# Kernel optimization log

Measured on AMD Instinct MI355X. Metric: run time of the kernel, lower is better.

## Reference

```python
import jax, jax.numpy as jnp
import numpy as np

B, S, D = 8, 8192, 512
E, DFF = 16, 512
CAPACITY = 2


def setup_inputs() -> dict:
    key = jax.random.key(0)
    ks = jax.random.split(key, 4)
    x = jax.random.normal(ks[0], (B, S, D), dtype=jnp.float32)
    gate_weight = jax.random.normal(ks[1], (D, E), dtype=jnp.float32) * 0.006
    w1 = jax.random.normal(ks[2], (E, D, DFF), dtype=jnp.float32) * 0.02
    b1 = jnp.zeros((E, DFF), dtype=jnp.float32)
    w2 = jax.random.normal(ks[3], (E, DFF, D), dtype=jnp.float32) * 0.02
    b2 = jnp.zeros((E, D), dtype=jnp.float32)
    return {"x": x, "gate_weight": gate_weight, "w1": w1, "b1": b1, "w2": w2, "b2": b2}


def reference(x, gate_weight, w1, b1, w2, b2):
    Bx, Sx, Dx = x.shape
    num_experts = gate_weight.shape[1]
    k = Sx // num_experts * CAPACITY  # tokens per expert (capacity limit)

    # Router: softmax over experts, then each expert picks its top-k tokens.
    logits = jnp.einsum('bsd,de->bse', x, gate_weight)
    affinity = jax.nn.softmax(logits, axis=-1).transpose(0, 2, 1)  # [b, e, s]
    gating, index = jax.lax.top_k(affinity, k)  # [b, e, k] each

    # Dispatch: gather selected tokens per expert (== one-hot einsum in torch).
    x_in = jnp.take_along_axis(x[:, None, :, :], index[..., None], axis=2)  # [b, e, k, d]

    # Per-expert MLP (grouped GEMM over expert axis).
    h = jax.nn.gelu(jnp.einsum('bekd,edh->bekh', x_in, w1) + b1[None, :, None, :])
    x_e = jnp.einsum('bekh,ehd->bekd', h, w2) + b2[None, :, None, :]

    # Combine: weight by gate prob and scatter-add back to token positions.
    weighted = gating[..., None] * x_e  # [b, e, k, d]
    out = jnp.zeros_like(x)
    idx_flat = index.reshape(Bx, num_experts * k)
    vals_flat = weighted.reshape(Bx, num_experts * k, Dx)
    out = out.at[jnp.arange(Bx)[:, None], idx_flat].add(vals_flat)
    return out
```

## Files before the change

### kernel.cpp

```cpp
#include <hip/hip_runtime.h>
#include <hip/hip_bf16.h>

typedef __attribute__((ext_vector_type(8))) short short8;
typedef __attribute__((ext_vector_type(4))) float floatx4;
typedef __attribute__((ext_vector_type(4))) unsigned short ushort4_t;

#define B_    8
#define S_    8192
#define D_    512
#define E_    16
#define DFF_  512
#define KROW_ 1024

__device__ __forceinline__ float bf2f(unsigned short u) {
    return __uint_as_float(((unsigned int)u) << 16);
}
__device__ __forceinline__ unsigned short f2bf(float f) {
    unsigned int u = __float_as_uint(f);
    u += 0x7FFFu + ((u >> 16) & 1u);
    return (unsigned short)(u >> 16);
}
__device__ __forceinline__ float gelu_tanh(float v) {
    const float t = v * fmaf(0.0713548065f, v * v, 1.5957691216057308f);
    return v * __builtin_amdgcn_rcpf(1.0f + __expf(-t));
}

#define GLD16(g, l) __builtin_amdgcn_global_load_lds( \
    (const __attribute__((address_space(1))) void*)(g), \
    (__attribute__((address_space(3))) void*)(l), 16, 0, 0)

__global__ __launch_bounds__(256) void transpose_w_k(
    const float* __restrict__ w1, const float* __restrict__ w2,
    unsigned short* __restrict__ w1t, unsigned short* __restrict__ w2t)
{
    __shared__ unsigned short tile[32][33];
    const int e = blockIdx.z & 15;
    const float*    src = (blockIdx.z < 16) ? w1 : w2;
    unsigned short* dst = (blockIdx.z < 16) ? w1t : w2t;
    const int x0 = blockIdx.x * 32, y0 = blockIdx.y * 32;
    const int tx = threadIdx.x, ty = threadIdx.y;
    const size_t base = (size_t)e * 512 * 512;
#pragma unroll
    for (int i = 0; i < 4; ++i)
        tile[ty + 8 * i][tx] = f2bf(src[base + (size_t)(y0 + ty + 8 * i) * 512 + x0 + tx]);
    __syncthreads();
#pragma unroll
    for (int i = 0; i < 4; ++i)
        dst[base + (size_t)(x0 + ty + 8 * i) * 512 + y0 + tx] = tile[tx][ty + 8 * i];
}

__global__ __launch_bounds__(256) void router_k(
    const float* __restrict__ x,
    const float* __restrict__ gw,
    float* __restrict__ aff,
    unsigned short* __restrict__ xb)
{
    __shared__ float gws[D_ * E_];
    const int t = threadIdx.x;
    for (int i = t; i < D_ * E_; i += 256) gws[i] = gw[i];
    __syncthreads();

    const int tok = blockIdx.x * 256 + t;
    const float4* xr = (const float4*)(x + (size_t)tok * D_);
    short8* xw = (short8*)(xb + (size_t)tok * D_);
    float acc[E_];
#pragma unroll
    for (int e = 0; e < E_; ++e) acc[e] = 0.f;

    for (int d8 = 0; d8 < D_ / 8; ++d8) {
        float4 va = xr[2 * d8];
        float4 vb = xr[2 * d8 + 1];
        short8 o;
        o[0] = (short)f2bf(va.x); o[1] = (short)f2bf(va.y);
        o[2] = (short)f2bf(va.z); o[3] = (short)f2bf(va.w);
        o[4] = (short)f2bf(vb.x); o[5] = (short)f2bf(vb.y);
        o[6] = (short)f2bf(vb.z); o[7] = (short)f2bf(vb.w);
        xw[d8] = o;
#pragma unroll
        for (int q = 0; q < 8; ++q) {
            const float xv = (q < 4) ? (&va.x)[q] : (&vb.x)[q - 4];
            const float* g = &gws[(d8 * 8 + q) * E_];
#pragma unroll
            for (int e = 0; e < E_; ++e) acc[e] = fmaf(xv, g[e], acc[e]);
        }
    }
    float mx = acc[0];
#pragma unroll
    for (int e = 1; e < E_; ++e) mx = fmaxf(mx, acc[e]);
    float sm = 0.f;
#pragma unroll
    for (int e = 0; e < E_; ++e) { acc[e] = expf(acc[e] - mx); sm += acc[e]; }
    const float inv = 1.f / sm;
    const int b = tok >> 13, s = tok & (S_ - 1);
#pragma unroll
    for (int e = 0; e < E_; ++e)
        aff[((size_t)b * E_ + e) * S_ + s] = acc[e] * inv;
}

__global__ __launch_bounds__(1024) void topk_k(
    const float* __restrict__ aff, int* __restrict__ idxb, int* __restrict__ map)
{
    __shared__ unsigned int keys[S_];
    __shared__ unsigned int hist[4][257];
    __shared__ unsigned int wsum[16];
    __shared__ unsigned int sh_b, sh_above, sh_ctr;

    const int b = blockIdx.x >> 4, e = blockIdx.x & 15;
    const float* a = aff + ((size_t)b * E_ + e) * S_;
    const int t = threadIdx.x;
    const int lane = t & 63, wid = t >> 6;

    for (int i = t; i < S_; i += 1024) keys[i] = __float_as_uint(a[i]);
    if (t == 0) sh_ctr = 0;
    hist[t >> 8][t & 255] = 0;
    __syncthreads();

    unsigned int prefix = 0, need = KROW_;
#pragma unroll
    for (int lev = 0; lev < 4; ++lev) {
        const int shift = (lev == 0) ? 23 : (lev == 1) ? 15 : (lev == 2) ? 7 : 0;
        const unsigned int fmask = (lev == 3) ? 127u : 255u;
        const int sw = shift + ((lev == 3) ? 7 : 8);
        const unsigned int mask_hi = 0xFFFFFFFFu << sw;

        for (int i = t; i < S_; i += 1024) {
            unsigned int k = keys[i];
            if ((k & mask_hi) == prefix)
                atomicAdd(&hist[t >> 8][(k >> shift) & fmask], 1u);
        }
        __syncthreads();

        if (t < 64) {
            unsigned int s0 = 0, s1 = 0, s2 = 0, s3 = 0;
#pragma unroll
            for (int c = 0; c < 4; ++c) {
                s0 += hist[c][4 * t + 0]; s1 += hist[c][4 * t + 1];
                s2 += hist[c][4 * t + 2]; s3 += hist[c][4 * t + 3];
            }
            const unsigned int v3 = s3, v2 = s2 + v3, v1 = s1 + v2, v0 = s0 + v1;
            const unsigned int G = v0;
            unsigned int T = v0;
#pragma unroll
            for (int off = 1; off < 64; off <<= 1) {
                unsigned int u = (unsigned int)__shfl_down((int)T, off);
                if (lane + off < 64) T += u;
            }
            const unsigned int R = T - G;
            unsigned int Sv[5];
            Sv[0] = T; Sv[1] = v1 + R; Sv[2] = v2 + R; Sv[3] = v3 + R; Sv[4] = R;
#pragma unroll
            for (int k2 = 0; k2 < 4; ++k2)
                if (Sv[k2] >= need && Sv[k2 + 1] < need) {
                    sh_b = (unsigned int)(4 * t + k2);
                    sh_above = Sv[k2 + 1];
                }
        }
        __syncthreads();
        prefix |= sh_b << shift;
        need   -= sh_above;
        if (lev < 3) hist[t >> 8][t & 255] = 0;
        __syncthreads();
    }

    const unsigned int thr = prefix;
    const unsigned int need_eq = need;
    const unsigned int m_gt = KROW_ - need_eq;

    int* idxg = idxb + ((size_t)b * E_ + e) * KROW_;
    for (int i = t; i < S_; i += 1024) {
        unsigned int k = keys[i];
        if (k > thr) {
            unsigned int slot = atomicAdd(&sh_ctr, 1u);
            idxg[slot] = i;
            map[((size_t)b * S_ + i) * E_ + e] = (int)slot;
        }
    }
    unsigned int lt = 0;
    const int i0 = t * 8;
#pragma unroll
    for (int q = 0; q < 8; ++q) lt += (keys[i0 + q] == thr);
    unsigned int incl = lt;
#pragma unroll
    for (int off = 1; off < 64; off <<= 1) {
        unsigned int u = (unsigned int)__shfl_up((int)incl, off);
        if (lane >= off) incl += u;
    }
    if (lane == 63) wsum[wid] = incl;
    __syncthreads();
    if (t < 16) {
        unsigned int wv = wsum[t];
        unsigned int ex = wv;
#pragma unroll
        for (int off = 1; off < 16; off <<= 1) {
            unsigned int u = (unsigned int)__shfl_up((int)ex, off);
            if (lane >= off) ex += u;
        }
        wsum[t] = ex - wv;
    }
    __syncthreads();
    unsigned int r = (incl - lt) + wsum[wid];
#pragma unroll
    for (int q = 0; q < 8; ++q) {
        if (keys[i0 + q] == thr) {
            if (r < need_eq) {
                idxg[m_gt + r] = i0 + q;
                map[((size_t)b * S_ + (i0 + q)) * E_ + e] = (int)(m_gt + r);
            }
            r++;
        }
    }
}

__global__ __launch_bounds__(256) void gemm1_k(
    const unsigned short* __restrict__ xb,
    const unsigned short* __restrict__ w1t,
    const float* __restrict__ b1,
    const int* __restrict__ idxb,
    unsigned short* __restrict__ h,
    int b_base)
{
    __shared__ unsigned short As[2][128 * 32];
    __shared__ unsigned short Bs[2][128 * 32];
    const int e  = blockIdx.z & 15;
    const int bl = blockIdx.z >> 4;
    const int b  = b_base + bl;
    const int m0 = blockIdx.x * 128;
    const int n0 = blockIdx.y * 128;
    const int t = threadIdx.x;
    const int w = t >> 6, l = t & 63;
    const int r0 = t >> 2, c0 = (t & 3) * 8;

    const int* idxg = idxb + ((size_t)b * E_ + e) * KROW_;
    const int s0 = idxg[m0 + r0];
    const int s1 = idxg[m0 + 64 + r0];
    const unsigned short* a0 = xb + ((size_t)b * S_ + s0) * D_ + c0;
    const unsigned short* a1 = xb + ((size_t)b * S_ + s1) * D_ + c0;
    const unsigned short* g0 = w1t + ((size_t)e * DFF_ + n0 + r0) * D_ + c0;
    const unsigned short* g1 = w1t + ((size_t)e * DFF_ + n0 + 64 + r0) * D_ + c0;

    floatx4 acc[4][4];
#pragma unroll
    for (int i = 0; i < 4; ++i)
#pragma unroll
        for (int j = 0; j < 4; ++j) acc[i][j] = (floatx4){0.f, 0.f, 0.f, 0.f};

    const int wm = (w >> 1) * 64, wn = (w & 1) * 64;
    const int lane15 = l & 15, lk = (l >> 4) * 8;

    {
        unsigned short* asd = &As[0][w * 512];
        unsigned short* bsd = &Bs[0][w * 512];
        GLD16(a0, asd); GLD16(a1, asd + 2048);
        GLD16(g0, bsd); GLD16(g1, bsd + 2048);
    }
    __syncthreads();

#pragma unroll
    for (int kt = 0; kt < D_ / 32; ++kt) {
        const int cur = kt & 1;
        if (kt + 1 < D_ / 32) {
            const int k1 = (kt + 1) * 32;
            unsigned short* asd = &As[cur ^ 1][w * 512];
            unsigned short* bsd = &Bs[cur ^ 1][w * 512];
            GLD16(a0 + k1, asd); GLD16(a1 + k1, asd + 2048);
            GLD16(g0 + k1, bsd); GLD16(g1 + k1, bsd + 2048);
        }
        short8 af[4], bf[4];
#pragma unroll
        for (int i = 0; i < 4; ++i) af[i] = *(const short8*)&As[cur][(wm + i * 16 + lane15) * 32 + lk];
#pragma unroll
        for (int j = 0; j < 4; ++j) bf[j] = *(const short8*)&Bs[cur][(wn + j * 16 + lane15) * 32 + lk];
#pragma unroll
        for (int i = 0; i < 4; ++i)
#pragma unroll
            for (int j = 0; j < 4; ++j)
                acc[i][j] = __builtin_amdgcn_mfma_f32_16x16x32_bf16(af[i], bf[j], acc[i][j], 0, 0, 0);
        __syncthreads();
    }

    float biasv[4];
#pragma unroll
    for (int j = 0; j < 4; ++j) biasv[j] = b1[e * DFF_ + n0 + wn + j * 16 + lane15];

    const size_t hbase = ((size_t)bl * E_ + e) * KROW_ * DFF_;
#pragma unroll
    for (int i = 0; i < 4; ++i)
#pragma unroll
        for (int j = 0; j < 4; ++j) {
            const int n = n0 + wn + j * 16 + lane15;
#pragma unroll
            for (int r = 0; r < 4; ++r) {
                const int m = m0 + wm + i * 16 + (l >> 4) * 4 + r;
                h[hbase + (size_t)m * DFF_ + n] = f2bf(gelu_tanh(acc[i][j][r] + biasv[j]));
            }
        }
}

__global__ __launch_bounds__(256) void gemm2_k(
    const unsigned short* __restrict__ h,
    const unsigned short* __restrict__ w2t,
    const float* __restrict__ b2,
    unsigned short* __restrict__ ex)
{
    __shared__ unsigned short As[2][128 * 32];
    __shared__ unsigned short Bs[2][128 * 32];
    const int e  = blockIdx.z & 15;
    const int bl = blockIdx.z >> 4;
    const int m0 = blockIdx.x * 128;
    const int n0 = blockIdx.y * 128;
    const int t = threadIdx.x;
    const int w = t >> 6, l = t & 63;
    const int r0 = t >> 2, c0 = (t & 3) * 8;

    const unsigned short* a0 = h + (((size_t)bl * E_ + e) * KROW_ + m0 + r0) * DFF_ + c0;
    const unsigned short* a1 = h + (((size_t)bl * E_ + e) * KROW_ + m0 + 64 + r0) * DFF_ + c0;
    const unsigned short* g0 = w2t + ((size_t)e * D_ + n0 + r0) * DFF_ + c0;
    const unsigned short* g1 = w2t + ((size_t)e * D_ + n0 + 64 + r0) * DFF_ + c0;

    floatx4 acc[4][4];
#pragma unroll
    for (int i = 0; i < 4; ++i)
#pragma unroll
        for (int j = 0; j < 4; ++j) acc[i][j] = (floatx4){0.f, 0.f, 0.f, 0.f};

    const int wm = (w >> 1) * 64, wn = (w & 1) * 64;
    const int lane15 = l & 15, lk = (l >> 4) * 8;

    {
        unsigned short* asd = &As[0][w * 512];
        unsigned short* bsd = &Bs[0][w * 512];
        GLD16(a0, asd); GLD16(a1, asd + 2048);
        GLD16(g0, bsd); GLD16(g1, bsd + 2048);
    }
    __syncthreads();

#pragma unroll
    for (int kt = 0; kt < DFF_ / 32; ++kt) {
        const int cur = kt & 1;
        if (kt + 1 < DFF_ / 32) {
            const int k1 = (kt + 1) * 32;
            unsigned short* asd = &As[cur ^ 1][w * 512];
            unsigned short* bsd = &Bs[cur ^ 1][w * 512];
            GLD16(a0 + k1, asd); GLD16(a1 + k1, asd + 2048);
            GLD16(g0 + k1, bsd); GLD16(g1 + k1, bsd + 2048);
        }
        short8 af[4], bf[4];
#pragma unroll
        for (int i = 0; i < 4; ++i) af[i] = *(const short8*)&As[cur][(wm + i * 16 + lane15) * 32 + lk];
#pragma unroll
        for (int j = 0; j < 4; ++j) bf[j] = *(const short8*)&Bs[cur][(wn + j * 16 + lane15) * 32 + lk];
#pragma unroll
        for (int i = 0; i < 4; ++i)
#pragma unroll
            for (int j = 0; j < 4; ++j)
                acc[i][j] = __builtin_amdgcn_mfma_f32_16x16x32_bf16(af[i], bf[j], acc[i][j], 0, 0, 0);
        __syncthreads();
    }

    float biasv[4];
#pragma unroll
    for (int j = 0; j < 4; ++j) biasv[j] = b2[e * D_ + n0 + wn + j * 16 + lane15];

    const size_t xbase = ((size_t)bl * E_ + e) * KROW_ * D_;
#pragma unroll
    for (int i = 0; i < 4; ++i)
#pragma unroll
        for (int j = 0; j < 4; ++j) {
            const int n = n0 + wn + j * 16 + lane15;
#pragma unroll
            for (int r = 0; r < 4; ++r) {
                const int m = m0 + wm + i * 16 + (l >> 4) * 4 + r;
                ex[xbase + (size_t)m * D_ + n] = f2bf(acc[i][j][r] + biasv[j]);
            }
        }
}

__global__ __launch_bounds__(256) void combine_k(
    const unsigned short* __restrict__ ex, const float* __restrict__ aff,
    const int* __restrict__ map, float* __restrict__ out, int b_base)
{
    const int t = threadIdx.x;
    const int w = t >> 6, l = t & 63;
    const size_t tokl = (size_t)blockIdx.x * 4 + w;
    const int bl = (int)(tokl >> 13);
    const int s  = (int)(tokl & (S_ - 1));
    const int b  = b_base + bl;

    int jv = -1; float gv = 0.f;
    if (l < 16) {
        jv = map[((size_t)b * S_ + s) * E_ + l];
        gv = aff[((size_t)b * E_ + l) * S_ + s];
    }
    float acc[8] = {0.f, 0.f, 0.f, 0.f, 0.f, 0.f, 0.f, 0.f};
#pragma unroll
    for (int e = 0; e < E_; ++e) {
        const int je = __shfl(jv, e);
        if (je < 0) continue;
        const float ge = __shfl(gv, e);
        const unsigned short* row = ex + (((size_t)bl * E_ + e) * KROW_ + je) * D_ + l * 8;
        short8 v = *(const short8*)row;
#pragma unroll
        for (int q = 0; q < 8; ++q) acc[q] += ge * bf2f((unsigned short)v[q]);
    }
    float* orow = out + ((size_t)b * S_ + s) * D_ + l * 8;
    float4 o0 = {acc[0], acc[1], acc[2], acc[3]};
    float4 o1 = {acc[4], acc[5], acc[6], acc[7]};
    ((float4*)orow)[0] = o0;
    ((float4*)orow)[1] = o1;
}

extern "C" void kernel_launch(void* const* d_in, const int* in_sizes, int n_in,
                              void* d_out, int out_size, void* d_ws, size_t ws_size,
                              hipStream_t stream) {
    const float* x  = (const float*)d_in[0];
    const float* gw = (const float*)d_in[1];
    const float* w1 = (const float*)d_in[2];
    const float* b1 = (const float*)d_in[3];
    const float* w2 = (const float*)d_in[4];
    const float* b2 = (const float*)d_in[5];
    float* out = (float*)d_out;
    char* ws = (char*)d_ws;

    size_t off = 0;
    float* aff = (float*)(ws + off);          off += (size_t)B_ * E_ * S_ * 4;
    int* idxb  = (int*)(ws + off);            off += (size_t)B_ * E_ * KROW_ * 4;
    int* map   = (int*)(ws + off);            off += (size_t)B_ * S_ * E_ * 4;
    unsigned short* w1t = (unsigned short*)(ws + off); off += (size_t)E_ * DFF_ * D_ * 2;
    unsigned short* w2t = (unsigned short*)(ws + off); off += (size_t)E_ * D_ * DFF_ * 2;
    unsigned short* xb  = (unsigned short*)(ws + off); off += (size_t)B_ * S_ * D_ * 2;
    const size_t fixed = off;
    const size_t per_b_h  = (size_t)E_ * KROW_ * DFF_ * 2;
    const size_t per_b_ex = (size_t)E_ * KROW_ * D_ * 2;
    const size_t per_b = per_b_h + per_b_ex;

    int bchunk = 1;
    if (ws_size > fixed + per_b) {
        size_t m = (ws_size - fixed) / per_b;
        bchunk = (int)(m > (size_t)B_ ? (size_t)B_ : m);
        if (bchunk < 1) bchunk = 1;
    }
    unsigned short* h  = (unsigned short*)(ws + fixed);
    unsigned short* ex = (unsigned short*)(ws + fixed + (size_t)bchunk * per_b_h);

    hipMemsetAsync(map, 0xFF, (size_t)B_ * S_ * E_ * 4, stream);
    transpose_w_k<<<dim3(16, 16, 32), dim3(32, 8, 1), 0, stream>>>(w1, w2, w1t, w2t);
    router_k<<<dim3((B_ * S_) / 256), dim3(256), 0, stream>>>(x, gw, aff, xb);
    topk_k<<<dim3(B_ * E_), dim3(1024), 0, stream>>>(aff, idxb, map);

    for (int b0 = 0; b0 < B_; b0 += bchunk) {
        const int bc = (b0 + bchunk <= B_) ? bchunk : (B_ - b0);
        gemm1_k<<<dim3(KROW_ / 128, DFF_ / 128, bc * E_), dim3(256), 0, stream>>>(
            xb, w1t, b1, idxb, h, b0);
        gemm2_k<<<dim3(KROW_ / 128, D_ / 128, bc * E_), dim3(256), 0, stream>>>(
            h, w2t, b2, ex);
        combine_k<<<dim3(bc * (S_ / 4)), dim3(256), 0, stream>>>(ex, aff, map, out, b0);
    }
}
```

Measured before the change: 599.7 us.

## Split router across 8 lanes per token and move bf16 conversion to separate kernel

The router now assigns 8 lanes per token, each accumulating two expert logits, and does the softmax max and sum with wave shuffles. This raises thread-level parallelism and cuts per-thread register pressure. The x-to-bf16 conversion is moved into its own fully coalesced elementwise kernel. In exchange, x is read from global memory twice and there is one extra kernel launch.

New measurement: 605.0 us. Within noise of the previous version (+0.9%).

```diff
diff --git a/kernel.cpp b/kernel.cpp
--- a/kernel.cpp
+++ b/kernel.cpp
@@ -28,6 +28,21 @@
 #define GLD16(g, l) __builtin_amdgcn_global_load_lds( \
     (const __attribute__((address_space(1))) void*)(g), \
     (__attribute__((address_space(3))) void*)(l), 16, 0, 0)
+
+__global__ __launch_bounds__(256) void cvt_x_k(
+    const float* __restrict__ x, unsigned short* __restrict__ xb, int n8)
+{
+    int i = blockIdx.x * 256 + threadIdx.x;
+    if (i >= n8) return;
+    float4 va = ((const float4*)x)[2 * i];
+    float4 vb = ((const float4*)x)[2 * i + 1];
+    short8 o;
+    o[0] = (short)f2bf(va.x); o[1] = (short)f2bf(va.y);
+    o[2] = (short)f2bf(va.z); o[3] = (short)f2bf(va.w);
+    o[4] = (short)f2bf(vb.x); o[5] = (short)f2bf(vb.y);
+    o[6] = (short)f2bf(vb.z); o[7] = (short)f2bf(vb.w);
+    ((short8*)xb)[i] = o;
+}
 
 __global__ __launch_bounds__(256) void transpose_w_k(
     const float* __restrict__ w1, const float* __restrict__ w2,
@@ -49,52 +64,57 @@
         dst[base + (size_t)(x0 + ty + 8 * i) * 512 + y0 + tx] = tile[tx][ty + 8 * i];
 }
 
-__global__ __launch_bounds__(256) void router_k(
+__global__ __launch_bounds__(512) void router_k(
     const float* __restrict__ x,
     const float* __restrict__ gw,
-    float* __restrict__ aff,
-    unsigned short* __restrict__ xb)
+    float* __restrict__ aff)
 {
     __shared__ float gws[D_ * E_];
     const int t = threadIdx.x;
-    for (int i = t; i < D_ * E_; i += 256) gws[i] = gw[i];
-    __syncthreads();
-
-    const int tok = blockIdx.x * 256 + t;
+    for (int i = t; i < D_ * E_; i += 512) gws[i] = gw[i];
+    __syncthreads();
+
+    const int lane = t & 63;
+    const int sub  = lane & 7;
+    const int tok  = blockIdx.x * 64 + (t >> 3);
     const float4* xr = (const float4*)(x + (size_t)tok * D_);
-    short8* xw = (short8*)(xb + (size_t)tok * D_);
-    float acc[E_];
-#pragma unroll
-    for (int e = 0; e < E_; ++e) acc[e] = 0.f;
-
+
+    float acc0 = 0.f, acc1 = 0.f;
+#pragma unroll 4
     for (int d8 = 0; d8 < D_ / 8; ++d8) {
-        float4 va = xr[2 * d8];
-        float4 vb = xr[2 * d8 + 1];
-        short8 o;
-        o[0] = (short)f2bf(va.x); o[1] = (short)f2bf(va.y);
-        o[2] = (short)f2bf(va.z); o[3] = (short)f2bf(va.w);
-        o[4] = (short)f2bf(vb.x); o[5] = (short)f2bf(vb.y);
-        o[6] = (short)f2bf(vb.z); o[7] = (short)f2bf(vb.w);
-        xw[d8] = o;
+        const float4 va = xr[2 * d8];
+        const float4 vb = xr[2 * d8 + 1];
 #pragma unroll
         for (int q = 0; q < 8; ++q) {
             const float xv = (q < 4) ? (&va.x)[q] : (&vb.x)[q - 4];
-            const float* g = &gws[(d8 * 8 + q) * E_];
-#pragma unroll
-            for (int e = 0; e < E_; ++e) acc[e] = fmaf(xv, g[e], acc[e]);
-        }
-    }
-    float mx = acc[0];
-#pragma unroll
-    for (int e = 1; e < E_; ++e) mx = fmaxf(mx, acc[e]);
+            const float2 gv = *(const float2*)&gws[(d8 * 8 + q) * E_ + 2 * sub];
+            acc0 = fmaf(xv, gv.x, acc0);
+            acc1 = fmaf(xv, gv.y, acc1);
+        }
+    }
+
+    const int base = lane & 56;
+    float accs[E_];
+#pragma unroll
+    for (int i = 0; i < 8; ++i) {
+        accs[2 * i]     = __shfl(acc0, base + i);
+        accs[2 * i + 1] = __shfl(acc1, base + i);
+    }
+    float mx = accs[0];
+#pragma unroll
+    for (int e = 1; e < E_; ++e) mx = fmaxf(mx, accs[e]);
+    const float e0v = expf(acc0 - mx);
+    const float e1v = expf(acc1 - mx);
     float sm = 0.f;
 #pragma unroll
-    for (int e = 0; e < E_; ++e) { acc[e] = expf(acc[e] - mx); sm += acc[e]; }
+    for (int i = 0; i < 8; ++i) {
+        sm += __shfl(e0v, base + i);
+        sm += __shfl(e1v, base + i);
+    }
     const float inv = 1.f / sm;
     const int b = tok >> 13, s = tok & (S_ - 1);
-#pragma unroll
-    for (int e = 0; e < E_; ++e)
-        aff[((size_t)b * E_ + e) * S_ + s] = acc[e] * inv;
+    aff[((size_t)b * E_ + 2 * sub) * S_ + s]     = e0v * inv;
+    aff[((size_t)b * E_ + 2 * sub + 1) * S_ + s] = e1v * inv;
 }
 
 __global__ __launch_bounds__(1024) void topk_k(
@@ -443,8 +463,10 @@
     unsigned short* ex = (unsigned short*)(ws + fixed + (size_t)bchunk * per_b_h);
 
     hipMemsetAsync(map, 0xFF, (size_t)B_ * S_ * E_ * 4, stream);
+    cvt_x_k<<<dim3((B_ * S_ * D_ / 8 + 255) / 256), dim3(256), 0, stream>>>(
+        x, xb, B_ * S_ * D_ / 8);
     transpose_w_k<<<dim3(16, 16, 32), dim3(32, 8, 1), 0, stream>>>(w1, w2, w1t, w2t);
-    router_k<<<dim3((B_ * S_) / 256), dim3(256), 0, stream>>>(x, gw, aff, xb);
+    router_k<<<dim3((B_ * S_) / 64), dim3(512), 0, stream>>>(x, gw, aff);
     topk_k<<<dim3(B_ * E_), dim3(1024), 0, stream>>>(aff, idxb, map);
 
     for (int b0 = 0; b0 < B_; b0 += bchunk) {
```
